# Performance work log

Measured on AMD Instinct MI355X. Metric: run time of the kernel, lower is better.

The kernel has to match this reference:

```python
import jax, jax.numpy as jnp
import numpy as np

T, N, F_IN, F_H, E = 16, 10000, 32, 64, 160000


def setup_inputs() -> dict:
    key = jax.random.key(0)
    ks = jax.random.split(key, 6)
    x = jax.random.normal(ks[0], (T, N, F_IN), dtype=jnp.float32)
    edge_index = jax.random.randint(ks[1], (2, E), 0, N, dtype=jnp.int64)
    edge_weight = jax.random.uniform(ks[2], (E,), dtype=jnp.float32)
    missing_mask = jnp.zeros((T, N, F_IN), dtype=jnp.bool_)
    # GCNConv params (glorot-ish init, zero bias as in PyG defaults)
    W1 = jax.random.normal(ks[3], (F_IN, F_H), dtype=jnp.float32) / np.float32(np.sqrt(F_IN))
    b1 = jnp.zeros((F_H,), dtype=jnp.float32)
    W2 = jax.random.normal(ks[4], (F_H, F_IN), dtype=jnp.float32) / np.float32(np.sqrt(F_H))
    b2 = jnp.zeros((F_IN,), dtype=jnp.float32)
    return dict(x=x, edge_index=edge_index, edge_weight=edge_weight,
                missing_mask=missing_mask, W1=W1, b1=b1, W2=W2, b2=b2)


def _gcn_norm(edge_index, edge_weight, num_nodes):
    # add self-loops with weight 1, symmetric normalization D^-1/2 (A+I) D^-1/2
    loop = jnp.arange(num_nodes, dtype=edge_index.dtype)
    src = jnp.concatenate([edge_index[0], loop])
    dst = jnp.concatenate([edge_index[1], loop])
    w = jnp.concatenate([edge_weight, jnp.ones((num_nodes,), edge_weight.dtype)])
    deg = jax.ops.segment_sum(w, dst, num_segments=num_nodes)
    dis = jnp.where(deg > 0, jax.lax.rsqrt(jnp.where(deg > 0, deg, 1.0)), 0.0)
    norm = dis[src] * w * dis[dst]
    return src, dst, norm


def _gcn_conv(x, src, dst, norm, W, b):
    # x: (T, N, Fin) -> (T, N, Fout); linear first, then gather-scale-scatter
    xw = jnp.einsum('tnf,fg->tng', x, W)
    msgs = xw[:, src, :] * norm[None, :, None]          # (T, E+N, Fout)
    out = jnp.zeros((x.shape[0], x.shape[1], W.shape[1]), x.dtype)
    out = out.at[:, dst, :].add(msgs)
    return out + b


def reference(x, edge_index, edge_weight, missing_mask, W1, b1, W2, b2):
    num_nodes = x.shape[1]
    src, dst, norm = _gcn_norm(edge_index, edge_weight, num_nodes)
    h = jax.nn.relu(_gcn_conv(x, src, dst, norm, W1, b1))
    out = _gcn_conv(h, src, dst, norm, W2, b2)
    return (out, 0)
```

## Files before the change

kernel.cpp:

```cpp
#include <hip/hip_runtime.h>
#include <hip/hip_bf16.h>

#define T_DIM   16
#define N_NODES 10000
#define FIN     32
#define FH      64
#define NE      160000
#define GPB     8
#define TB      2
#define NCHUNK  (T_DIM / TB)
#define NF      (N_NODES * FIN)

__global__ void build_deg_kernel(const int* __restrict__ ei,
                                 const float* __restrict__ w,
                                 float* __restrict__ deg,
                                 int* __restrict__ cnt,
                                 int* __restrict__ slot) {
    int e = blockIdx.x * blockDim.x + threadIdx.x;
    if (e < NE) {
        int d = ei[NE + e];
        atomicAdd(&deg[d], w[e]);
        slot[e] = atomicAdd(&cnt[d], 1);
    }
}

__global__ __launch_bounds__(1024) void mid_kernel(
    const float* __restrict__ deg, float* __restrict__ dis,
    float* __restrict__ selfn,
    const int* __restrict__ cnt, int* __restrict__ rowptr,
    const float* __restrict__ W1, const float* __restrict__ W2,
    float2* __restrict__ W1p, float2* __restrict__ W2p) {
    __shared__ int sm[1024];
    int b = blockIdx.x;
    int tid = threadIdx.x;
    if (b < 10) {
        int n = b * 1024 + tid;
        if (n < N_NODES) {
            float d = deg[n] + 1.0f;
            float r = rsqrtf(d);
            dis[n] = r;
            selfn[n] = r * r;
        }
    } else if (b == 10) {
        int base = tid * 10;
        int v[10];
        int s = 0;
#pragma unroll
        for (int k = 0; k < 10; ++k) {
            int i = base + k;
            v[k] = (i < N_NODES) ? cnt[i] : 0;
            s += v[k];
        }
        sm[tid] = s;
        __syncthreads();
        for (int off = 1; off < 1024; off <<= 1) {
            int t = (tid >= off) ? sm[tid - off] : 0;
            __syncthreads();
            sm[tid] += t;
            __syncthreads();
        }
        int run = (tid > 0) ? sm[tid - 1] : 0;
#pragma unroll
        for (int k = 0; k < 10; ++k) {
            int i = base + k;
            if (i <= N_NODES) rowptr[i] = run;
            run += v[k];
        }
    } else if (b == 11) {
        int f = tid >> 5, l = tid & 31;
        W1p[tid] = make_float2(W1[f * FH + l], W1[f * FH + 32 + l]);
    } else {
        int j = tid >> 5, l = tid & 31;
        W2p[tid] = make_float2(W2[j * FIN + l], W2[(j + 32) * FIN + l]);
    }
}

__global__ void build_csr_kernel(const int* __restrict__ ei,
                                 const float* __restrict__ w,
                                 const float* __restrict__ dis,
                                 const int* __restrict__ rowptr,
                                 const int* __restrict__ slot,
                                 int2* __restrict__ edges) {
    int e = blockIdx.x * blockDim.x + threadIdx.x;
    if (e < NE) {
        int s = ei[e];
        int d = ei[NE + e];
        int pos = rowptr[d] + slot[e];
        edges[pos] = make_int2(s, __float_as_int(dis[s] * w[e] * dis[d]));
    }
}

__global__ __launch_bounds__(256) void layer1_kernel(
    const float* __restrict__ x,
    const int* __restrict__ rowptr,
    const int2* __restrict__ edges,
    const float* __restrict__ selfn,
    const float2* __restrict__ W1p,
    const float* __restrict__ b1,
    const float2* __restrict__ W2p,
    float2* __restrict__ gp) {
    __shared__ float2 sW1p[FIN * 32];
    __shared__ float2 sW2p[32 * FIN];
    __shared__ float sB1[FH];
    __shared__ float sAcc[GPB][TB][FIN];
    __shared__ float sH[GPB][TB][FH];

    int tid = threadIdx.x;
#pragma unroll
    for (int i = 0; i < 4; ++i) sW1p[tid + i * 256] = W1p[tid + i * 256];
#pragma unroll
    for (int i = 0; i < 4; ++i) sW2p[tid + i * 256] = W2p[tid + i * 256];
    if (tid < FH) sB1[tid] = b1[tid];
    __syncthreads();

    int b = blockIdx.x;
    int tc = b & (NCHUNK - 1);
    int nb = b >> 3;
    int grp = tid >> 5;
    int lane = tid & 31;
    int n = nb * GPB + grp;

    const float* x0 = x + (size_t)(tc * TB) * NF;

    float sn = selfn[n];
    float a0 = sn * x0[n * FIN + lane];
    float a1 = sn * x0[NF + n * FIN + lane];

    int e = rowptr[n], e1 = rowptr[n + 1];
    for (; e + 4 <= e1; e += 4) {
        int2 p0 = edges[e], p1 = edges[e + 1], p2 = edges[e + 2], p3 = edges[e + 3];
        int c0 = p0.x * FIN + lane, c1 = p1.x * FIN + lane;
        int c2 = p2.x * FIN + lane, c3 = p3.x * FIN + lane;
        float x00 = x0[c0], x01 = x0[NF + c0];
        float x10 = x0[c1], x11 = x0[NF + c1];
        float x20 = x0[c2], x21 = x0[NF + c2];
        float x30 = x0[c3], x31 = x0[NF + c3];
        float v0 = __int_as_float(p0.y), v1 = __int_as_float(p1.y);
        float v2 = __int_as_float(p2.y), v3 = __int_as_float(p3.y);
        a0 = fmaf(v0, x00, a0); a1 = fmaf(v0, x01, a1);
        a0 = fmaf(v1, x10, a0); a1 = fmaf(v1, x11, a1);
        a0 = fmaf(v2, x20, a0); a1 = fmaf(v2, x21, a1);
        a0 = fmaf(v3, x30, a0); a1 = fmaf(v3, x31, a1);
    }
    for (; e < e1; ++e) {
        int2 p = edges[e];
        float v = __int_as_float(p.y);
        int c = p.x * FIN + lane;
        a0 = fmaf(v, x0[c], a0);
        a1 = fmaf(v, x0[NF + c], a1);
    }

    sAcc[grp][0][lane] = a0;
    sAcc[grp][1][lane] = a1;
    float h0 = sB1[lane];
    float h1 = sB1[lane + 32];
    float h2 = h0, h3 = h1;
#pragma unroll
    for (int f = 0; f < FIN; ++f) {
        float2 w = sW1p[f * 32 + lane];
        float af0 = sAcc[grp][0][f];
        float af1 = sAcc[grp][1][f];
        h0 = fmaf(af0, w.x, h0); h1 = fmaf(af0, w.y, h1);
        h2 = fmaf(af1, w.x, h2); h3 = fmaf(af1, w.y, h3);
    }
    sH[grp][0][lane] = fmaxf(h0, 0.0f);
    sH[grp][0][lane + 32] = fmaxf(h1, 0.0f);
    sH[grp][1][lane] = fmaxf(h2, 0.0f);
    sH[grp][1][lane + 32] = fmaxf(h3, 0.0f);
    float g0 = 0.0f, g1 = 0.0f;
#pragma unroll
    for (int j = 0; j < 32; ++j) {
        float2 w = sW2p[j * 32 + lane];
        g0 = fmaf(sH[grp][0][j], w.x, g0);
        g0 = fmaf(sH[grp][0][j + 32], w.y, g0);
        g1 = fmaf(sH[grp][1][j], w.x, g1);
        g1 = fmaf(sH[grp][1][j + 32], w.y, g1);
    }
    gp[(size_t)tc * (N_NODES * 32) + n * 32 + lane] = make_float2(g0, g1);
}

__global__ __launch_bounds__(256) void layer2_kernel(
    const float2* __restrict__ gp,
    const int* __restrict__ rowptr,
    const int2* __restrict__ edges,
    const float* __restrict__ selfn,
    const float* __restrict__ b2,
    float* __restrict__ out, int out_size) {
    int b = blockIdx.x;
    int tc = b & (NCHUNK - 1);
    int nb = b >> 3;
    int tid = threadIdx.x;
    int grp = tid >> 5;
    int lane = tid & 31;
    int n = nb * GPB + grp;

    const float2* gq = gp + (size_t)tc * (N_NODES * 32) + lane;

    float sn = selfn[n];
    float bb = b2[lane];
    float2 gs = gq[n * 32];
    float a0 = fmaf(sn, gs.x, bb);
    float a1 = fmaf(sn, gs.y, bb);

    int e = rowptr[n], e1 = rowptr[n + 1];
    for (; e + 4 <= e1; e += 4) {
        int2 p0 = edges[e], p1 = edges[e + 1], p2 = edges[e + 2], p3 = edges[e + 3];
        float2 q0 = gq[p0.x * 32], q1 = gq[p1.x * 32];
        float2 q2 = gq[p2.x * 32], q3 = gq[p3.x * 32];
        float v0 = __int_as_float(p0.y), v1 = __int_as_float(p1.y);
        float v2 = __int_as_float(p2.y), v3 = __int_as_float(p3.y);
        a0 = fmaf(v0, q0.x, a0); a1 = fmaf(v0, q0.y, a1);
        a0 = fmaf(v1, q1.x, a0); a1 = fmaf(v1, q1.y, a1);
        a0 = fmaf(v2, q2.x, a0); a1 = fmaf(v2, q2.y, a1);
        a0 = fmaf(v3, q3.x, a0); a1 = fmaf(v3, q3.y, a1);
    }
    for (; e < e1; ++e) {
        int2 p = edges[e];
        float v = __int_as_float(p.y);
        float2 q = gq[p.x * 32];
        a0 = fmaf(v, q.x, a0);
        a1 = fmaf(v, q.y, a1);
    }

    int t0 = tc * TB;
    out[(size_t)t0 * NF + n * FIN + lane] = a0;
    out[(size_t)t0 * NF + NF + n * FIN + lane] = a1;

    if (b == 0 && tid == 0) {
        for (int i = T_DIM * NF; i < out_size; ++i) out[i] = 0.0f;
    }
}

extern "C" void kernel_launch(void* const* d_in, const int* in_sizes, int n_in,
                              void* d_out, int out_size, void* d_ws, size_t ws_size,
                              hipStream_t stream) {
    const float* x  = (const float*)d_in[0];
    const int*   ei = (const int*)d_in[1];
    const float* w  = (const float*)d_in[2];
    const float* W1 = (const float*)d_in[4];
    const float* b1 = (const float*)d_in[5];
    const float* W2 = (const float*)d_in[6];
    const float* b2 = (const float*)d_in[7];
    float* out = (float*)d_out;

    char* p = (char*)d_ws;
    float2* gp    = (float2*)p; p += sizeof(float2) * (size_t)N_NODES * NCHUNK * 32;
    float* deg    = (float*)p; p += sizeof(float) * N_NODES;
    int*   cnt    = (int*)p;   p += sizeof(int) * N_NODES;
    float* dis    = (float*)p; p += sizeof(float) * N_NODES;
    float* selfn  = (float*)p; p += sizeof(float) * N_NODES;
    int*   rowptr = (int*)p;   p += sizeof(int) * (N_NODES + 1);
    int*   slot   = (int*)p;   p += sizeof(int) * NE;
    int2*  edges  = (int2*)p;  p += sizeof(int2) * NE;
    float2* W1p   = (float2*)p; p += sizeof(float2) * FIN * 32;
    float2* W2p   = (float2*)p; p += sizeof(float2) * 32 * FIN;

    hipMemsetAsync(deg, 0, sizeof(float) * N_NODES * 2, stream);

    build_deg_kernel<<<(NE + 255) / 256, 256, 0, stream>>>(ei, w, deg, cnt, slot);
    mid_kernel<<<13, 1024, 0, stream>>>(deg, dis, selfn, cnt, rowptr,
                                        W1, W2, W1p, W2p);
    build_csr_kernel<<<(NE + 255) / 256, 256, 0, stream>>>(ei, w, dis, rowptr,
                                                           slot, edges);
    layer1_kernel<<<(N_NODES / GPB) * NCHUNK, 256, 0, stream>>>(
        x, rowptr, edges, selfn, W1p, b1, W2p, gp);
    layer2_kernel<<<(N_NODES / GPB) * NCHUNK, 256, 0, stream>>>(
        gp, rowptr, edges, selfn, b2, out, out_size);
}
```

Baseline: 228.0 us.

## Pre-interleave input timesteps into float2 layout and enlarge layer1 blocks

Adds a transpose kernel that packs the two timesteps of each chunk into interleaved float2 records, so layer1's neighbour gathers become one 8-byte load per lane instead of two 4-byte loads from separate planes. Layer1 also moves to 512-thread blocks holding 16 nodes each, which halves the per-block cost of staging the weight matrices into shared memory. The price is an extra kernel launch and a full extra read and write of x (about 20 MB), plus higher shared-memory and register pressure per block.

```diff
diff --git a/kernel.cpp b/kernel.cpp
--- a/kernel.cpp
+++ b/kernel.cpp
@@ -6,7 +6,6 @@
 #define FIN     32
 #define FH      64
 #define NE      160000
-#define GPB     8
 #define TB      2
 #define NCHUNK  (T_DIM / TB)
 #define NF      (N_NODES * FIN)
@@ -90,8 +89,21 @@
     }
 }
 
-__global__ __launch_bounds__(256) void layer1_kernel(
-    const float* __restrict__ x,
+__global__ __launch_bounds__(256) void transpose_kernel(
+    const float* __restrict__ x, float2* __restrict__ xp) {
+    int b = blockIdx.x;
+    int tc = b & (NCHUNK - 1);
+    int nb = b >> 3;
+    int grp = threadIdx.x >> 5;
+    int lane = threadIdx.x & 31;
+    int n = nb * 8 + grp;
+    const float* x0 = x + (size_t)(tc * TB) * NF + n * FIN + lane;
+    xp[(size_t)tc * (N_NODES * 32) + n * 32 + lane] = make_float2(x0[0], x0[NF]);
+}
+
+#define GPB1 16
+__global__ __launch_bounds__(512) void layer1_kernel(
+    const float2* __restrict__ xp,
     const int* __restrict__ rowptr,
     const int2* __restrict__ edges,
     const float* __restrict__ selfn,
@@ -102,14 +114,14 @@
     __shared__ float2 sW1p[FIN * 32];
     __shared__ float2 sW2p[32 * FIN];
     __shared__ float sB1[FH];
-    __shared__ float sAcc[GPB][TB][FIN];
-    __shared__ float sH[GPB][TB][FH];
+    __shared__ float sAcc[GPB1][TB][FIN];
+    __shared__ float sH[GPB1][TB][FH];
 
     int tid = threadIdx.x;
 #pragma unroll
-    for (int i = 0; i < 4; ++i) sW1p[tid + i * 256] = W1p[tid + i * 256];
-#pragma unroll
-    for (int i = 0; i < 4; ++i) sW2p[tid + i * 256] = W2p[tid + i * 256];
+    for (int i = 0; i < 2; ++i) sW1p[tid + i * 512] = W1p[tid + i * 512];
+#pragma unroll
+    for (int i = 0; i < 2; ++i) sW2p[tid + i * 512] = W2p[tid + i * 512];
     if (tid < FH) sB1[tid] = b1[tid];
     __syncthreads();
 
@@ -118,36 +130,33 @@
     int nb = b >> 3;
     int grp = tid >> 5;
     int lane = tid & 31;
-    int n = nb * GPB + grp;
-
-    const float* x0 = x + (size_t)(tc * TB) * NF;
+    int n = nb * GPB1 + grp;
+
+    const float2* xq = xp + (size_t)tc * (N_NODES * 32) + lane;
 
     float sn = selfn[n];
-    float a0 = sn * x0[n * FIN + lane];
-    float a1 = sn * x0[NF + n * FIN + lane];
+    float2 xs = xq[n * 32];
+    float a0 = sn * xs.x;
+    float a1 = sn * xs.y;
 
     int e = rowptr[n], e1 = rowptr[n + 1];
     for (; e + 4 <= e1; e += 4) {
         int2 p0 = edges[e], p1 = edges[e + 1], p2 = edges[e + 2], p3 = edges[e + 3];
-        int c0 = p0.x * FIN + lane, c1 = p1.x * FIN + lane;
-        int c2 = p2.x * FIN + lane, c3 = p3.x * FIN + lane;
-        float x00 = x0[c0], x01 = x0[NF + c0];
-        float x10 = x0[c1], x11 = x0[NF + c1];
-        float x20 = x0[c2], x21 = x0[NF + c2];
-        float x30 = x0[c3], x31 = x0[NF + c3];
+        float2 q0 = xq[p0.x * 32], q1 = xq[p1.x * 32];
+        float2 q2 = xq[p2.x * 32], q3 = xq[p3.x * 32];
         float v0 = __int_as_float(p0.y), v1 = __int_as_float(p1.y);
         float v2 = __int_as_float(p2.y), v3 = __int_as_float(p3.y);
-        a0 = fmaf(v0, x00, a0); a1 = fmaf(v0, x01, a1);
-        a0 = fmaf(v1, x10, a0); a1 = fmaf(v1, x11, a1);
-        a0 = fmaf(v2, x20, a0); a1 = fmaf(v2, x21, a1);
-        a0 = fmaf(v3, x30, a0); a1 = fmaf(v3, x31, a1);
+        a0 = fmaf(v0, q0.x, a0); a1 = fmaf(v0, q0.y, a1);
+        a0 = fmaf(v1, q1.x, a0); a1 = fmaf(v1, q1.y, a1);
+        a0 = fmaf(v2, q2.x, a0); a1 = fmaf(v2, q2.y, a1);
+        a0 = fmaf(v3, q3.x, a0); a1 = fmaf(v3, q3.y, a1);
     }
     for (; e < e1; ++e) {
         int2 p = edges[e];
         float v = __int_as_float(p.y);
-        int c = p.x * FIN + lane;
-        a0 = fmaf(v, x0[c], a0);
-        a1 = fmaf(v, x0[NF + c], a1);
+        float2 q = xq[p.x * 32];
+        a0 = fmaf(v, q.x, a0);
+        a1 = fmaf(v, q.y, a1);
     }
 
     sAcc[grp][0][lane] = a0;
@@ -192,7 +201,7 @@
     int tid = threadIdx.x;
     int grp = tid >> 5;
     int lane = tid & 31;
-    int n = nb * GPB + grp;
+    int n = nb * 8 + grp;
 
     const float2* gq = gp + (size_t)tc * (N_NODES * 32) + lane;
 
@@ -244,6 +253,7 @@
     float* out = (float*)d_out;
 
     char* p = (char*)d_ws;
+    float2* xp    = (float2*)p; p += sizeof(float2) * (size_t)N_NODES * NCHUNK * 32;
     float2* gp    = (float2*)p; p += sizeof(float2) * (size_t)N_NODES * NCHUNK * 32;
     float* deg    = (float*)p; p += sizeof(float) * N_NODES;
     int*   cnt    = (int*)p;   p += sizeof(int) * N_NODES;
@@ -262,8 +272,9 @@
                                         W1, W2, W1p, W2p);
     build_csr_kernel<<<(NE + 255) / 256, 256, 0, stream>>>(ei, w, dis, rowptr,
                                                            slot, edges);
-    layer1_kernel<<<(N_NODES / GPB) * NCHUNK, 256, 0, stream>>>(
-        x, rowptr, edges, selfn, W1p, b1, W2p, gp);
-    layer2_kernel<<<(N_NODES / GPB) * NCHUNK, 256, 0, stream>>>(
+    transpose_kernel<<<(N_NODES / 8) * NCHUNK, 256, 0, stream>>>(x, xp);
+    layer1_kernel<<<(N_NODES / GPB1) * NCHUNK, 512, 0, stream>>>(
+        xp, rowptr, edges, selfn, W1p, b1, W2p, gp);
+    layer2_kernel<<<(N_NODES / 8) * NCHUNK, 256, 0, stream>>>(
         gp, rowptr, edges, selfn, b2, out, out_size);
 }
```

New measurement: 237.0 us. +4.0%, slower.

## Interleave four timesteps into float4 records for wider gathers

Applied to the files above, without the earlier changes.

Adds a prep pass that transposes x into per-node float4 records holding four timesteps, padded to 33 entries per node. The degree-count work is merged into the same launch. Both layer kernels now gather one float4 per edge instead of two scalars or a float2, which halves the number of edge-list walks (TB goes from 2 to 4). The intermediate buffer uses the same packed layout. Blocks grow to 512 threads covering 16 nodes each. The cost is an extra full pass over x and a larger workspace, and more registers per thread.

```diff
diff --git a/kernel.cpp b/kernel.cpp
--- a/kernel.cpp
+++ b/kernel.cpp
@@ -6,21 +6,33 @@
 #define FIN     32
 #define FH      64
 #define NE      160000
-#define GPB     8
-#define TB      2
+#define TB      4
 #define NCHUNK  (T_DIM / TB)
 #define NF      (N_NODES * FIN)
-
-__global__ void build_deg_kernel(const int* __restrict__ ei,
-                                 const float* __restrict__ w,
-                                 float* __restrict__ deg,
-                                 int* __restrict__ cnt,
-                                 int* __restrict__ slot) {
-    int e = blockIdx.x * blockDim.x + threadIdx.x;
-    if (e < NE) {
-        int d = ei[NE + e];
-        atomicAdd(&deg[d], w[e]);
-        slot[e] = atomicAdd(&cnt[d], 1);
+#define RECQ    33
+#define GPB     16
+
+__global__ __launch_bounds__(256) void prep_kernel(
+    const float* __restrict__ x, float4* __restrict__ xp4,
+    const int* __restrict__ ei, const float* __restrict__ w,
+    float* __restrict__ deg, int* __restrict__ cnt, int* __restrict__ slot) {
+    int b = blockIdx.x;
+    int tid = threadIdx.x;
+    if (b < 5000) {
+        int tc = b & 3;
+        int nb = b >> 2;
+        int f = tid & 31, ns = tid >> 5;
+        int n = nb * 8 + ns;
+        const float* xb = x + (size_t)(tc * TB) * NF + n * FIN + f;
+        float4 v = make_float4(xb[0], xb[NF], xb[2 * NF], xb[3 * NF]);
+        xp4[(size_t)tc * (N_NODES * RECQ) + n * RECQ + f] = v;
+    } else {
+        int e = (b - 5000) * 256 + tid;
+        if (e < NE) {
+            int d = ei[NE + e];
+            atomicAdd(&deg[d], w[e]);
+            slot[e] = atomicAdd(&cnt[d], 1);
+        }
     }
 }
 
@@ -90,143 +102,126 @@
     }
 }
 
-__global__ __launch_bounds__(256) void layer1_kernel(
-    const float* __restrict__ x,
+#define GF4(P, Q) { float4 q = Q[(size_t)(P).x * RECQ];                     \
+                    float vv = __int_as_float((P).y);                       \
+                    a0 = fmaf(vv, q.x, a0); a1 = fmaf(vv, q.y, a1);         \
+                    a2 = fmaf(vv, q.z, a2); a3 = fmaf(vv, q.w, a3); }
+
+#define GATHER4(Q)                                                          \
+    for (; e + 4 <= e1; e += 4) {                                           \
+        int2 p0 = edges[e], p1 = edges[e + 1];                              \
+        int2 p2 = edges[e + 2], p3 = edges[e + 3];                          \
+        GF4(p0, Q) GF4(p1, Q) GF4(p2, Q) GF4(p3, Q)                         \
+    }                                                                       \
+    for (; e < e1; ++e) { int2 p = edges[e]; GF4(p, Q) }
+
+__global__ __launch_bounds__(512) void layer1_kernel(
+    const float4* __restrict__ xp4,
     const int* __restrict__ rowptr,
     const int2* __restrict__ edges,
     const float* __restrict__ selfn,
     const float2* __restrict__ W1p,
     const float* __restrict__ b1,
     const float2* __restrict__ W2p,
-    float2* __restrict__ gp) {
+    float4* __restrict__ gp4) {
     __shared__ float2 sW1p[FIN * 32];
     __shared__ float2 sW2p[32 * FIN];
     __shared__ float sB1[FH];
-    __shared__ float sAcc[GPB][TB][FIN];
-    __shared__ float sH[GPB][TB][FH];
-
-    int tid = threadIdx.x;
-#pragma unroll
-    for (int i = 0; i < 4; ++i) sW1p[tid + i * 256] = W1p[tid + i * 256];
-#pragma unroll
-    for (int i = 0; i < 4; ++i) sW2p[tid + i * 256] = W2p[tid + i * 256];
+    __shared__ float2 sAcc[GPB][FIN];
+    __shared__ float sH[GPB][TB / 2][FH];
+
+    int tid = threadIdx.x;
+    sW1p[tid] = W1p[tid];
+    sW1p[tid + 512] = W1p[tid + 512];
+    sW2p[tid] = W2p[tid];
+    sW2p[tid + 512] = W2p[tid + 512];
     if (tid < FH) sB1[tid] = b1[tid];
     __syncthreads();
 
-    int b = blockIdx.x;
-    int tc = b & (NCHUNK - 1);
-    int nb = b >> 3;
+    int bck = blockIdx.x;
+    int tc = bck & 3;
+    int nb = bck >> 2;
     int grp = tid >> 5;
     int lane = tid & 31;
     int n = nb * GPB + grp;
 
-    const float* x0 = x + (size_t)(tc * TB) * NF;
+    const float4* xq = xp4 + (size_t)tc * (N_NODES * RECQ) + lane;
 
     float sn = selfn[n];
-    float a0 = sn * x0[n * FIN + lane];
-    float a1 = sn * x0[NF + n * FIN + lane];
+    float4 xs = xq[(size_t)n * RECQ];
+    float a0 = sn * xs.x, a1 = sn * xs.y, a2 = sn * xs.z, a3 = sn * xs.w;
 
     int e = rowptr[n], e1 = rowptr[n + 1];
-    for (; e + 4 <= e1; e += 4) {
-        int2 p0 = edges[e], p1 = edges[e + 1], p2 = edges[e + 2], p3 = edges[e + 3];
-        int c0 = p0.x * FIN + lane, c1 = p1.x * FIN + lane;
-        int c2 = p2.x * FIN + lane, c3 = p3.x * FIN + lane;
-        float x00 = x0[c0], x01 = x0[NF + c0];
-        float x10 = x0[c1], x11 = x0[NF + c1];
-        float x20 = x0[c2], x21 = x0[NF + c2];
-        float x30 = x0[c3], x31 = x0[NF + c3];
-        float v0 = __int_as_float(p0.y), v1 = __int_as_float(p1.y);
-        float v2 = __int_as_float(p2.y), v3 = __int_as_float(p3.y);
-        a0 = fmaf(v0, x00, a0); a1 = fmaf(v0, x01, a1);
-        a0 = fmaf(v1, x10, a0); a1 = fmaf(v1, x11, a1);
-        a0 = fmaf(v2, x20, a0); a1 = fmaf(v2, x21, a1);
-        a0 = fmaf(v3, x30, a0); a1 = fmaf(v3, x31, a1);
-    }
-    for (; e < e1; ++e) {
-        int2 p = edges[e];
-        float v = __int_as_float(p.y);
-        int c = p.x * FIN + lane;
-        a0 = fmaf(v, x0[c], a0);
-        a1 = fmaf(v, x0[NF + c], a1);
-    }
-
-    sAcc[grp][0][lane] = a0;
-    sAcc[grp][1][lane] = a1;
-    float h0 = sB1[lane];
-    float h1 = sB1[lane + 32];
-    float h2 = h0, h3 = h1;
-#pragma unroll
-    for (int f = 0; f < FIN; ++f) {
-        float2 w = sW1p[f * 32 + lane];
-        float af0 = sAcc[grp][0][f];
-        float af1 = sAcc[grp][1][f];
-        h0 = fmaf(af0, w.x, h0); h1 = fmaf(af0, w.y, h1);
-        h2 = fmaf(af1, w.x, h2); h3 = fmaf(af1, w.y, h3);
-    }
-    sH[grp][0][lane] = fmaxf(h0, 0.0f);
-    sH[grp][0][lane + 32] = fmaxf(h1, 0.0f);
-    sH[grp][1][lane] = fmaxf(h2, 0.0f);
-    sH[grp][1][lane + 32] = fmaxf(h3, 0.0f);
-    float g0 = 0.0f, g1 = 0.0f;
-#pragma unroll
-    for (int j = 0; j < 32; ++j) {
-        float2 w = sW2p[j * 32 + lane];
-        g0 = fmaf(sH[grp][0][j], w.x, g0);
-        g0 = fmaf(sH[grp][0][j + 32], w.y, g0);
-        g1 = fmaf(sH[grp][1][j], w.x, g1);
-        g1 = fmaf(sH[grp][1][j + 32], w.y, g1);
-    }
-    gp[(size_t)tc * (N_NODES * 32) + n * 32 + lane] = make_float2(g0, g1);
-}
-
-__global__ __launch_bounds__(256) void layer2_kernel(
-    const float2* __restrict__ gp,
+    GATHER4(xq)
+
+    float gt0, gt1, gt2, gt3;
+#pragma unroll
+    for (int r = 0; r < 2; ++r) {
+        float aA = (r == 0) ? a0 : a2;
+        float aB = (r == 0) ? a1 : a3;
+        sAcc[grp][lane] = make_float2(aA, aB);
+        float h0 = sB1[lane];
+        float h1 = sB1[lane + 32];
+        float h2 = h0, h3 = h1;
+#pragma unroll
+        for (int f = 0; f < FIN; ++f) {
+            float2 w = sW1p[f * 32 + lane];
+            float2 af = sAcc[grp][f];
+            h0 = fmaf(af.x, w.x, h0); h1 = fmaf(af.x, w.y, h1);
+            h2 = fmaf(af.y, w.x, h2); h3 = fmaf(af.y, w.y, h3);
+        }
+        sH[grp][0][lane] = fmaxf(h0, 0.0f);
+        sH[grp][0][lane + 32] = fmaxf(h1, 0.0f);
+        sH[grp][1][lane] = fmaxf(h2, 0.0f);
+        sH[grp][1][lane + 32] = fmaxf(h3, 0.0f);
+        float g0 = 0.0f, g1 = 0.0f;
+#pragma unroll
+        for (int j = 0; j < 32; ++j) {
+            float2 w = sW2p[j * 32 + lane];
+            g0 = fmaf(sH[grp][0][j], w.x, g0);
+            g0 = fmaf(sH[grp][0][j + 32], w.y, g0);
+            g1 = fmaf(sH[grp][1][j], w.x, g1);
+            g1 = fmaf(sH[grp][1][j + 32], w.y, g1);
+        }
+        if (r == 0) { gt0 = g0; gt1 = g1; } else { gt2 = g0; gt3 = g1; }
+    }
+    gp4[(size_t)tc * (N_NODES * RECQ) + n * RECQ + lane] =
+        make_float4(gt0, gt1, gt2, gt3);
+}
+
+__global__ __launch_bounds__(512) void layer2_kernel(
+    const float4* __restrict__ gp4,
     const int* __restrict__ rowptr,
     const int2* __restrict__ edges,
     const float* __restrict__ selfn,
     const float* __restrict__ b2,
     float* __restrict__ out, int out_size) {
-    int b = blockIdx.x;
-    int tc = b & (NCHUNK - 1);
-    int nb = b >> 3;
+    int bck = blockIdx.x;
+    int tc = bck & 3;
+    int nb = bck >> 2;
     int tid = threadIdx.x;
     int grp = tid >> 5;
     int lane = tid & 31;
     int n = nb * GPB + grp;
 
-    const float2* gq = gp + (size_t)tc * (N_NODES * 32) + lane;
+    const float4* gq = gp4 + (size_t)tc * (N_NODES * RECQ) + lane;
 
     float sn = selfn[n];
     float bb = b2[lane];
-    float2 gs = gq[n * 32];
-    float a0 = fmaf(sn, gs.x, bb);
-    float a1 = fmaf(sn, gs.y, bb);
+    float4 gs = gq[(size_t)n * RECQ];
+    float a0 = fmaf(sn, gs.x, bb), a1 = fmaf(sn, gs.y, bb);
+    float a2 = fmaf(sn, gs.z, bb), a3 = fmaf(sn, gs.w, bb);
 
     int e = rowptr[n], e1 = rowptr[n + 1];
-    for (; e + 4 <= e1; e += 4) {
-        int2 p0 = edges[e], p1 = edges[e + 1], p2 = edges[e + 2], p3 = edges[e + 3];
-        float2 q0 = gq[p0.x * 32], q1 = gq[p1.x * 32];
-        float2 q2 = gq[p2.x * 32], q3 = gq[p3.x * 32];
-        float v0 = __int_as_float(p0.y), v1 = __int_as_float(p1.y);
-        float v2 = __int_as_float(p2.y), v3 = __int_as_float(p3.y);
-        a0 = fmaf(v0, q0.x, a0); a1 = fmaf(v0, q0.y, a1);
-        a0 = fmaf(v1, q1.x, a0); a1 = fmaf(v1, q1.y, a1);
-        a0 = fmaf(v2, q2.x, a0); a1 = fmaf(v2, q2.y, a1);
-        a0 = fmaf(v3, q3.x, a0); a1 = fmaf(v3, q3.y, a1);
-    }
-    for (; e < e1; ++e) {
-        int2 p = edges[e];
-        float v = __int_as_float(p.y);
-        float2 q = gq[p.x * 32];
-        a0 = fmaf(v, q.x, a0);
-        a1 = fmaf(v, q.y, a1);
-    }
-
-    int t0 = tc * TB;
-    out[(size_t)t0 * NF + n * FIN + lane] = a0;
-    out[(size_t)t0 * NF + NF + n * FIN + lane] = a1;
-
-    if (b == 0 && tid == 0) {
+    GATHER4(gq)
+
+    float* ob = out + (size_t)(tc * TB) * NF + n * FIN + lane;
+    ob[0] = a0;
+    ob[NF] = a1;
+    ob[2 * NF] = a2;
+    ob[3 * NF] = a3;
+
+    if (bck == 0 && tid == 0) {
         for (int i = T_DIM * NF; i < out_size; ++i) out[i] = 0.0f;
     }
 }
@@ -244,7 +239,8 @@
     float* out = (float*)d_out;
 
     char* p = (char*)d_ws;
-    float2* gp    = (float2*)p; p += sizeof(float2) * (size_t)N_NODES * NCHUNK * 32;
+    float4* xp4   = (float4*)p; p += sizeof(float4) * (size_t)N_NODES * RECQ * NCHUNK;
+    float4* gp4   = (float4*)p; p += sizeof(float4) * (size_t)N_NODES * RECQ * NCHUNK;
     float* deg    = (float*)p; p += sizeof(float) * N_NODES;
     int*   cnt    = (int*)p;   p += sizeof(int) * N_NODES;
     float* dis    = (float*)p; p += sizeof(float) * N_NODES;
@@ -257,13 +253,14 @@
 
     hipMemsetAsync(deg, 0, sizeof(float) * N_NODES * 2, stream);
 
-    build_deg_kernel<<<(NE + 255) / 256, 256, 0, stream>>>(ei, w, deg, cnt, slot);
+    prep_kernel<<<5000 + (NE + 255) / 256, 256, 0, stream>>>(
+        x, xp4, ei, w, deg, cnt, slot);
     mid_kernel<<<13, 1024, 0, stream>>>(deg, dis, selfn, cnt, rowptr,
                                         W1, W2, W1p, W2p);
     build_csr_kernel<<<(NE + 255) / 256, 256, 0, stream>>>(ei, w, dis, rowptr,
                                                            slot, edges);
-    layer1_kernel<<<(N_NODES / GPB) * NCHUNK, 256, 0, stream>>>(
-        x, rowptr, edges, selfn, W1p, b1, W2p, gp);
-    layer2_kernel<<<(N_NODES / GPB) * NCHUNK, 256, 0, stream>>>(
-        gp, rowptr, edges, selfn, b2, out, out_size);
-}
+    layer1_kernel<<<(N_NODES / GPB) * NCHUNK, 512, 0, stream>>>(
+        xp4, rowptr, edges, selfn, W1p, b1, W2p, gp4);
+    layer2_kernel<<<(N_NODES / GPB) * NCHUNK, 512, 0, stream>>>(
+        gp4, rowptr, edges, selfn, b2, out, out_size);
+}
```

Measured after the change: 253.9 us. +11.4%, slower.
